# Kernel tuning notes

Hardware: AMD Instinct MI355X
Metric: run time of the kernel (lower is better)

Reference implementation:

```python
import jax, jax.numpy as jnp
import numpy as np

B, T, D, H = 2, 2048, 1024, 16
DK = D // H


def setup_inputs() -> dict:
    key = jax.random.key(0)
    ks = jax.random.split(key, 13)
    s = 1.0 / np.sqrt(D)
    return {
        "q": jax.random.normal(ks[0], (B, T, D), jnp.float32),
        "k": jax.random.normal(ks[1], (B, T, D), jnp.float32),
        "v": jax.random.normal(ks[2], (B, T, D), jnp.float32),
        "mask": jax.random.randint(ks[3], (B, T, T), 0, 2, jnp.int32),
        "Wq": jax.random.normal(ks[4], (D, D), jnp.float32) * s,
        "bq": jax.random.normal(ks[5], (D,), jnp.float32) * s,
        "Wk": jax.random.normal(ks[6], (D, D), jnp.float32) * s,
        "bk": jax.random.normal(ks[7], (D,), jnp.float32) * s,
        "Wv": jax.random.normal(ks[8], (D, D), jnp.float32) * s,
        "bv": jax.random.normal(ks[9], (D,), jnp.float32) * s,
        "Wo": jax.random.normal(ks[10], (D, D), jnp.float32) * s,
        "bo": jax.random.normal(ks[11], (D,), jnp.float32) * s,
    }


def reference(q, k, v, mask, Wq, bq, Wk, bk, Wv, bv, Wo, bo):
    # Linear projections (torch Linear: x @ W.T + b), split into heads.
    Q = (q @ Wq.T + bq).reshape(B, T, H, DK).transpose(0, 2, 1, 3)  # [B,H,Tq,dk]
    K = (k @ Wk.T + bk).reshape(B, T, H, DK).transpose(0, 2, 1, 3)
    V = (v @ Wv.T + bv).reshape(B, T, H, DK).transpose(0, 2, 1, 3)
    scores = jnp.einsum("bhqd,bhkd->bhqk", Q, K) / jnp.sqrt(jnp.float32(DK))
    # 3-dim mask path: mask==0 -> -1e9, broadcast over heads.
    scores = jnp.where(mask[:, None, :, :] == 0, jnp.float32(-1e9), scores)
    attn = jax.nn.softmax(scores, axis=-1)
    out = jnp.einsum("bhqk,bhkd->bhqd", attn, V)  # [B,H,Tq,dk]
    out = out.transpose(0, 2, 1, 3).reshape(B, T, D)
    return out @ Wo.T + bo
```

## Files before the change

### kernel.cpp

```cpp
#include <hip/hip_runtime.h>
#include <cstdint>
#include <cstddef>

#define TSEQ 2048
#define DMOD 1024
#define NHEAD 16
#define NBATCH 2
#define MT (NBATCH * TSEQ)
#define LOG2E 1.44269504088896340736f

typedef __attribute__((ext_vector_type(8))) __bf16 bf16x8;
typedef __attribute__((ext_vector_type(4))) float f32x4;
typedef __attribute__((ext_vector_type(8))) unsigned short u16x8;
typedef __attribute__((ext_vector_type(4))) unsigned short u16x4;
typedef __attribute__((ext_vector_type(4))) uint32_t u32x4;

__device__ __forceinline__ unsigned short f2bf(float f) {
  uint32_t u = __builtin_bit_cast(uint32_t, f);
  u += 0x7fffu + ((u >> 16) & 1u);
  return (unsigned short)(u >> 16);
}

__device__ __forceinline__ uint32_t cvt_pk_bf16(float a, float b) {
  uint32_t r;
  asm("v_cvt_pk_bf16_f32 %0, %1, %2" : "=v"(r) : "v"(a), "v"(b));
  return r;
}

__device__ __forceinline__ void gload_lds16(const void* g, const void* l) {
  auto gp = (const __attribute__((address_space(1))) uint32_t*)((uintptr_t)g);
  auto lp = (__attribute__((address_space(3))) uint32_t*)((uintptr_t)l);
  __builtin_amdgcn_global_load_lds(gp, lp, 16, 0, 0);
}

__global__ __launch_bounds__(256) void cvt_wm(const float* __restrict__ w0,
                                              const float* __restrict__ w1,
                                              const float* __restrict__ w2,
                                              const float* __restrict__ w3,
                                              const int* __restrict__ m,
                                              unsigned short* __restrict__ dw,
                                              uint32_t* __restrict__ mx) {
  const int bx = blockIdx.x;
  if (bx < 4096) {
    const size_t idx = ((size_t)bx * 256 + threadIdx.x) * 4;
    const int wsel = (int)(idx >> 20);
    const float* s = wsel == 0 ? w0 : (wsel == 1 ? w1 : (wsel == 2 ? w2 : w3));
    const float4 t = *(const float4*)(s + (idx & 0xFFFFFu));
    u16x4 o;
    o[0] = f2bf(t.x); o[1] = f2bf(t.y); o[2] = f2bf(t.z); o[3] = f2bf(t.w);
    *(u16x4*)(dw + idx) = o;
  } else {
    const size_t W = (size_t)(bx - 4096) * 256 + threadIdx.x;
    const int hi = (int)((W >> 3) & 3), ct = (int)(W & 7);
    const size_t bqkt = W >> 5;
    const int kt = (int)(bqkt & 15);
    const size_t bq = bqkt >> 4;
    const int4 mm = *(const int4*)(m + bq * TSEQ + kt * 128 + ct * 16 + hi * 4);
    const uint32_t o = (mm.x ? 0xFFu : 0u) | (mm.y ? 0xFF00u : 0u) |
                       (mm.z ? 0xFF0000u : 0u) | (mm.w ? 0xFF000000u : 0u);
    mx[W] = o;
  }
}

__device__ __forceinline__ void store_c(unsigned short* C, size_t idx, float v) { C[idx] = f2bf(v); }
__device__ __forceinline__ void store_c(float* C, size_t idx, float v) { C[idx] = v; }

template <typename OT, int MF, bool AF32>
__global__ __launch_bounds__(256) void gemm_bt(const void* __restrict__ A0v,
                                               const void* __restrict__ A1v,
                                               const void* __restrict__ A2v,
                                               const unsigned short* __restrict__ W0,
                                               const unsigned short* __restrict__ W1,
                                               const unsigned short* __restrict__ W2,
                                               const float* __restrict__ b0,
                                               const float* __restrict__ b1,
                                               const float* __restrict__ b2,
                                               OT* __restrict__ C0, OT* __restrict__ C1, OT* __restrict__ C2,
                                               float s0, float s1, float s2) {
  constexpr int BM = MF * 32;
  constexpr int NX = 4096 / BM;
  const int nb = gridDim.x, per = nb >> 3, bid = blockIdx.x;
  const int swz = (bid & 7) * per + (bid >> 3);
  const int z = swz / (NX * 8);
  const int rem = swz % (NX * 8);
  const int m0 = (rem >> 3) * BM, n0 = (rem & 7) * 128;

  const void* Av = z == 0 ? A0v : (z == 1 ? A1v : A2v);
  const unsigned short* Bw = z == 0 ? W0 : (z == 1 ? W1 : W2);
  const float* bias = z == 0 ? b0 : (z == 1 ? b1 : b2);
  OT* C = z == 0 ? C0 : (z == 1 ? C1 : C2);
  const float scale = z == 0 ? s0 : (z == 1 ? s1 : s2);

  __shared__ alignas(16) unsigned short As[2][BM * 64];
  __shared__ alignas(16) unsigned short Bs[2][128 * 64];
  const int tid = threadIdx.x;
  const int wid = tid >> 6;
  const int lane = tid & 63;
  const int lo = lane & 15, hi = lane >> 4;
  const int wr = wid >> 1, wc = wid & 1;
  f32x4 acc[MF][4] = {};

  float4 fa[MF][2];

  auto loadA = [&](int k0) {
    if constexpr (AF32) {
#pragma unroll
      for (int j = 0; j < MF; ++j) {
        const int chunk = j * 256 + tid;
        const int row = chunk >> 3, cl = (chunk & 7) ^ (row & 7);
        const float* p = (const float*)Av + (size_t)(m0 + row) * DMOD + k0 + cl * 8;
        fa[j][0] = *(const float4*)p;
        fa[j][1] = *(const float4*)(p + 4);
      }
    }
  };
  auto writeA = [&](int buf) {
    if constexpr (AF32) {
#pragma unroll
      for (int j = 0; j < MF; ++j) {
        const int chunk = j * 256 + tid;
        u32x4 o;
        o[0] = cvt_pk_bf16(fa[j][0].x, fa[j][0].y);
        o[1] = cvt_pk_bf16(fa[j][0].z, fa[j][0].w);
        o[2] = cvt_pk_bf16(fa[j][1].x, fa[j][1].y);
        o[3] = cvt_pk_bf16(fa[j][1].z, fa[j][1].w);
        *(u32x4*)((char*)As + buf * (BM * 128) + chunk * 16) = o;
      }
    }
  };
  auto stage = [&](int buf, int k0) {
    if constexpr (!AF32) {
#pragma unroll
      for (int i = 0; i < MF; ++i) {
        const int chunk = i * 256 + tid;
        const int row = chunk >> 3, cl = (chunk & 7) ^ (row & 7);
        gload_lds16((const unsigned short*)Av + (size_t)(m0 + row) * DMOD + k0 + cl * 8,
                    (const char*)As + buf * (BM * 128) + chunk * 16);
      }
    }
#pragma unroll
    for (int i = 0; i < 4; ++i) {
      const int chunk = i * 256 + tid;
      const int row = chunk >> 3, cl = (chunk & 7) ^ (row & 7);
      gload_lds16(Bw + (size_t)(n0 + row) * DMOD + k0 + cl * 8,
                  (const char*)Bs + buf * 16384 + chunk * 16);
    }
  };

  loadA(0);
  writeA(0);
  stage(0, 0);
  __syncthreads();

  for (int k0 = 0; k0 < DMOD; k0 += 64) {
    const int cur = (k0 >> 6) & 1;
    const bool more = k0 + 64 < DMOD;
    if (more) { loadA(k0 + 64); stage(cur ^ 1, k0 + 64); }

#pragma unroll
    for (int kk = 0; kk < 2; ++kk) {
      bf16x8 af[MF], bfr[4];
#pragma unroll
      for (int m = 0; m < MF; ++m) {
        const int row = wr * (MF * 16) + m * 16 + lo;
        af[m] = *(const bf16x8*)((const char*)As + cur * (BM * 128) +
                                 row * 128 + (((kk * 4 + hi) ^ (lo & 7)) * 16));
      }
#pragma unroll
      for (int n = 0; n < 4; ++n) {
        const int row = wc * 64 + n * 16 + lo;
        bfr[n] = *(const bf16x8*)((const char*)Bs + cur * 16384 +
                                  row * 128 + (((kk * 4 + hi) ^ (lo & 7)) * 16));
      }
#pragma unroll
      for (int m = 0; m < MF; ++m)
#pragma unroll
        for (int n = 0; n < 4; ++n)
          acc[m][n] = __builtin_amdgcn_mfma_f32_16x16x32_bf16(af[m], bfr[n], acc[m][n], 0, 0, 0);
    }

    if (more) writeA(cur ^ 1);
    __syncthreads();
  }

#pragma unroll
  for (int n = 0; n < 4; ++n) {
    const int col = n0 + wc * 64 + n * 16 + lo;
    const float bv = bias[col];
#pragma unroll
    for (int m = 0; m < MF; ++m) {
      const int row = m0 + wr * (MF * 16) + m * 16 + hi * 4;
#pragma unroll
      for (int r = 0; r < 4; ++r)
        store_c(C, (size_t)(row + r) * DMOD + col, (acc[m][n][r] + bv) * scale);
    }
  }
}

__global__ __launch_bounds__(256) void transpose_v(const unsigned short* __restrict__ Vp,
                                                   unsigned short* __restrict__ Vt) {
  __shared__ alignas(16) unsigned short tile[64][72];
  const int tid = threadIdx.x;
  const int bt0 = blockIdx.x * 64;
  const int h = blockIdx.y;
  const int b = bt0 >> 11;
  const int t0 = bt0 & (TSEQ - 1);
#pragma unroll
  for (int i = 0; i < 2; ++i) {
    const int chunk = i * 256 + tid;
    const int row = chunk >> 3, c = chunk & 7;
    *(uint4*)((char*)&tile[row][0] + c * 16) =
        *(const uint4*)(Vp + (size_t)(bt0 + row) * DMOD + h * 64 + c * 8);
  }
  __syncthreads();
#pragma unroll
  for (int i = 0; i < 2; ++i) {
    const int chunk = i * 256 + tid;
    const int dk = chunk >> 3, c = chunk & 7;
    u16x8 o;
#pragma unroll
    for (int j = 0; j < 8; ++j) {
      const int x = c * 8 + j;
      const int kl = (x & 32) | ((x & 24) >> 1) | ((x & 4) << 2) | (x & 3);
      o[j] = tile[kl][dk];
    }
    *(u16x8*)(Vt + ((size_t)(b * NHEAD + h) * 64 + dk) * TSEQ + t0 + c * 8) = o;
  }
}

__global__ __launch_bounds__(512, 4) void attn_kernel(const unsigned short* __restrict__ Qp,
                                                      const unsigned short* __restrict__ Kp,
                                                      const unsigned short* __restrict__ Vt,
                                                      const uint32_t* __restrict__ mx,
                                                      unsigned short* __restrict__ AO) {
  __shared__ alignas(16) unsigned short Ks[2][128 * 64];
  __shared__ alignas(16) unsigned short Vs[2][64 * 128];
  const int tid = threadIdx.x;
  const int w = tid >> 6, lane = tid & 63;
  const int lo = lane & 15, hi = lane >> 4;
  const int f = blockIdx.x;
  const int swz = (f & 7) * 64 + (f >> 3);
  const int q0 = (swz & 15) * 128;
  const int h = (swz >> 4) & 15;
  const int b = swz >> 8;

  bf16x8 qf[2];
  {
    const unsigned short* qsrc =
        Qp + (size_t)(b * TSEQ + q0 + w * 16 + lo) * DMOD + h * 64 + hi * 8;
    qf[0] = *(const bf16x8*)qsrc;
    qf[1] = *(const bf16x8*)(qsrc + 32);
  }

  bf16x8 ones;
  {
    u32x4 od;
    od[0] = 0x3F803F80u; od[1] = 0x3F803F80u; od[2] = 0x3F803F80u; od[3] = 0x3F803F80u;
    ones = __builtin_bit_cast(bf16x8, od);
  }

  f32x4 o_acc[4] = {};
  f32x4 l_acc = {};

  const size_t kbase = (size_t)(b * TSEQ) * DMOD + h * 64;
  const size_t vbase = (size_t)(b * NHEAD + h) * 64 * TSEQ;

  const int c0 = tid, c1 = 512 + tid;
  const unsigned short* kp0 = Kp + kbase + (size_t)(c0 >> 3) * DMOD + ((c0 & 7) ^ ((c0 >> 3) & 7)) * 8;
  const unsigned short* kp1 = Kp + kbase + (size_t)(c1 >> 3) * DMOD + ((c1 & 7) ^ ((c1 >> 3) & 7)) * 8;
  const unsigned short* vp0 = Vt + vbase + (size_t)(c0 >> 4) * TSEQ + ((c0 & 15) ^ ((c0 >> 4) & 7)) * 8;
  const unsigned short* vp1 = Vt + vbase + (size_t)(c1 >> 4) * TSEQ + ((c1 & 15) ^ ((c1 >> 4) & 7)) * 8;
  const uint32_t* mp = mx + (size_t)(b * TSEQ + q0 + w * 16 + lo) * 512 + hi * 8;
  const int wb0 = c0 * 16, wb1 = c1 * 16;

  int koffA[8], koffB[8];
#pragma unroll
  for (int ct = 0; ct < 8; ++ct) {
    const int kcol = ct * 16 + lo;
    koffA[ct] = kcol * 128 + ((hi ^ (kcol & 7)) * 16);
    koffB[ct] = kcol * 128 + (((4 + hi) ^ (kcol & 7)) * 16);
  }
  int voff[4][4];
#pragma unroll
  for (int vt = 0; vt < 4; ++vt) {
    const int dk = vt * 16 + lo;
#pragma unroll
    for (int c = 0; c < 4; ++c) voff[vt][c] = dk * 256 + (((c * 4 + hi) ^ (dk & 7)) * 16);
  }

  auto stage = [&](int buf) {
    gload_lds16(kp0, (const char*)Ks[buf] + wb0);
    gload_lds16(kp1, (const char*)Ks[buf] + wb1);
    gload_lds16(vp0, (const char*)Vs[buf] + wb0);
    gload_lds16(vp1, (const char*)Vs[buf] + wb1);
    kp0 += (size_t)128 * DMOD; kp1 += (size_t)128 * DMOD;
    vp0 += 128; vp1 += 128;
  };

  const uint32_t selA = 0x01010000u, selB = 0x03030202u;
  const int NT = TSEQ / 128;

  uint4 mc0 = *(const uint4*)mp, mc1 = *(const uint4*)(mp + 4);
  mp += 32;
  stage(0);
  __syncthreads();

  for (int kt = 0; kt < NT; ++kt) {
    uint4 mn0 = mc0, mn1 = mc1;
    if (kt + 1 < NT) {
      mn0 = *(const uint4*)mp;
      mn1 = *(const uint4*)(mp + 4);
      mp += 32;
      stage((kt + 1) & 1);
    }

    const char* ksb = (const char*)Ks[kt & 1];
    const char* vsb = (const char*)Vs[kt & 1];
    f32x4 s[8];
    __builtin_amdgcn_s_setprio(1);
#pragma unroll
    for (int ct = 0; ct < 8; ++ct) {
      bf16x8 kf0 = *(const bf16x8*)(ksb + koffA[ct]);
      bf16x8 kf1 = *(const bf16x8*)(ksb + koffB[ct]);
      f32x4 zz = {0.f, 0.f, 0.f, 0.f};
      s[ct] = __builtin_amdgcn_mfma_f32_16x16x32_bf16(kf0, qf[0], zz, 0, 0, 0);
      s[ct] = __builtin_amdgcn_mfma_f32_16x16x32_bf16(kf1, qf[1], s[ct], 0, 0, 0);
    }
    __builtin_amdgcn_s_setprio(0);

#pragma unroll
    for (int ct = 0; ct < 8; ++ct) {
      s[ct][0] = __builtin_exp2f(s[ct][0]);
      s[ct][1] = __builtin_exp2f(s[ct][1]);
      s[ct][2] = __builtin_exp2f(s[ct][2]);
      s[ct][3] = __builtin_exp2f(s[ct][3]);
    }

    bf16x8 pf[4];
#pragma unroll
    for (int c = 0; c < 4; ++c) {
      const uint32_t We = c == 0 ? mc0.x : (c == 1 ? mc0.z : (c == 2 ? mc1.x : mc1.z));
      const uint32_t Wo = c == 0 ? mc0.y : (c == 1 ? mc0.w : (c == 2 ? mc1.y : mc1.w));
      u32x4 pd;
      pd[0] = cvt_pk_bf16(s[2 * c][0], s[2 * c][1]) & __builtin_amdgcn_perm(We, We, selA);
      pd[1] = cvt_pk_bf16(s[2 * c][2], s[2 * c][3]) & __builtin_amdgcn_perm(We, We, selB);
      pd[2] = cvt_pk_bf16(s[2 * c + 1][0], s[2 * c + 1][1]) & __builtin_amdgcn_perm(Wo, Wo, selA);
      pd[3] = cvt_pk_bf16(s[2 * c + 1][2], s[2 * c + 1][3]) & __builtin_amdgcn_perm(Wo, Wo, selB);
      pf[c] = __builtin_bit_cast(bf16x8, pd);
    }

    __builtin_amdgcn_s_setprio(1);
#pragma unroll
    for (int vt = 0; vt < 4; ++vt) {
#pragma unroll
      for (int c = 0; c < 4; ++c) {
        bf16x8 vf = *(const bf16x8*)(vsb + voff[vt][c]);
        o_acc[vt] = __builtin_amdgcn_mfma_f32_16x16x32_bf16(pf[c], vf, o_acc[vt], 0, 0, 0);
      }
    }
#pragma unroll
    for (int c = 0; c < 4; ++c)
      l_acc = __builtin_amdgcn_mfma_f32_16x16x32_bf16(pf[c], ones, l_acc, 0, 0, 0);
    __builtin_amdgcn_s_setprio(0);

    __syncthreads();
    mc0 = mn0; mc1 = mn1;
  }

#pragma unroll
  for (int r = 0; r < 4; ++r) {
    const float rl = 1.0f / l_acc[r];
    const size_t orow = (size_t)(b * TSEQ + q0 + w * 16 + hi * 4 + r) * DMOD + h * 64;
#pragma unroll
    for (int vt = 0; vt < 4; ++vt)
      AO[orow + vt * 16 + lo] = f2bf(o_acc[vt][r] * rl);
  }
}

extern "C" void kernel_launch(void* const* d_in, const int* in_sizes, int n_in,
                              void* d_out, int out_size, void* d_ws, size_t ws_size,
                              hipStream_t stream) {
  const float* q  = (const float*)d_in[0];
  const float* k  = (const float*)d_in[1];
  const float* v  = (const float*)d_in[2];
  const int* mask = (const int*)d_in[3];
  const float* Wq = (const float*)d_in[4];
  const float* bq = (const float*)d_in[5];
  const float* Wk = (const float*)d_in[6];
  const float* bk = (const float*)d_in[7];
  const float* Wv = (const float*)d_in[8];
  const float* bv = (const float*)d_in[9];
  const float* Wo = (const float*)d_in[10];
  const float* bo = (const float*)d_in[11];
  float* out = (float*)d_out;

  char* ws = (char*)d_ws;
  const size_t SZ_BT = (size_t)MT * DMOD * 2;

  unsigned short* Qp  = (unsigned short*)(ws + 0);
  unsigned short* Kp  = (unsigned short*)(ws + SZ_BT);
  unsigned short* Vp  = (unsigned short*)(ws + 2 * SZ_BT);
  unsigned short* Vt  = (unsigned short*)(ws + 3 * SZ_BT);
  unsigned short* Wqb = (unsigned short*)(ws + 4 * SZ_BT);
  uint32_t*       mx  = (uint32_t*)(ws + 5 * SZ_BT);
  unsigned short* AO  = Vp;
  unsigned short* Wob = Wqb + 3 * DMOD * DMOD;

  const int nW = DMOD * DMOD;

  cvt_wm<<<dim3(4096 + (NBATCH * TSEQ * 16 * 32) / 256), 256, 0, stream>>>(
      Wq, Wk, Wv, Wo, mask, Wqb, mx);

  const float qs = 0.125f * LOG2E;
  gemm_bt<unsigned short, 4, true><<<dim3(768), 256, 0, stream>>>(
      q, k, v, Wqb, Wqb + nW, Wqb + 2 * nW, bq, bk, bv, Qp, Kp, Vp, qs, 1.0f, 1.0f);

  transpose_v<<<dim3(MT / 64, NHEAD), 256, 0, stream>>>(Vp, Vt);

  attn_kernel<<<dim3(512), 512, 0, stream>>>(Qp, Kp, Vt, mx, AO);

  gemm_bt<float, 2, false><<<dim3(512), 256, 0, stream>>>(
      AO, AO, AO, Wob, Wob, Wob, bo, bo, bo, out, out, out, 1.0f, 1.0f, 1.0f);
}
```

Baseline: 138.8 us.

## Software-pipeline QK of next tile with softmax/PV of current tile

New measurement: 194.0 us. 1.4x slower.

```diff
diff --git a/kernel.cpp b/kernel.cpp
--- a/kernel.cpp
+++ b/kernel.cpp
@@ -234,7 +234,7 @@
                                                       const uint32_t* __restrict__ mx,
                                                       unsigned short* __restrict__ AO) {
   __shared__ alignas(16) unsigned short Ks[2][128 * 64];
-  __shared__ alignas(16) unsigned short Vs[2][64 * 128];
+  __shared__ alignas(16) unsigned short Vs[3][64 * 128];
   const int tid = threadIdx.x;
   const int w = tid >> 6, lane = tid & 63;
   const int lo = lane & 15, hi = lane >> 4;
@@ -288,84 +288,103 @@
     for (int c = 0; c < 4; ++c) voff[vt][c] = dk * 256 + (((c * 4 + hi) ^ (dk & 7)) * 16);
   }
 
-  auto stage = [&](int buf) {
-    gload_lds16(kp0, (const char*)Ks[buf] + wb0);
-    gload_lds16(kp1, (const char*)Ks[buf] + wb1);
-    gload_lds16(vp0, (const char*)Vs[buf] + wb0);
-    gload_lds16(vp1, (const char*)Vs[buf] + wb1);
+  auto stage = [&](int kbuf, int vbuf) {
+    gload_lds16(kp0, (const char*)Ks[kbuf] + wb0);
+    gload_lds16(kp1, (const char*)Ks[kbuf] + wb1);
+    gload_lds16(vp0, (const char*)Vs[vbuf] + wb0);
+    gload_lds16(vp1, (const char*)Vs[vbuf] + wb1);
     kp0 += (size_t)128 * DMOD; kp1 += (size_t)128 * DMOD;
     vp0 += 128; vp1 += 128;
   };
 
   const uint32_t selA = 0x01010000u, selB = 0x03030202u;
+
+#define QK_TILE(S, KSB) do {                                                  \
+    const char* _k = (KSB);                                                   \
+    __builtin_amdgcn_s_setprio(1);                                            \
+    _Pragma("unroll")                                                         \
+    for (int ct = 0; ct < 8; ++ct) {                                          \
+      bf16x8 kf0 = *(const bf16x8*)(_k + koffA[ct]);                          \
+      bf16x8 kf1 = *(const bf16x8*)(_k + koffB[ct]);                          \
+      f32x4 zz = {0.f, 0.f, 0.f, 0.f};                                        \
+      S[ct] = __builtin_amdgcn_mfma_f32_16x16x32_bf16(kf0, qf[0], zz, 0, 0, 0);    \
+      S[ct] = __builtin_amdgcn_mfma_f32_16x16x32_bf16(kf1, qf[1], S[ct], 0, 0, 0); \
+    }                                                                         \
+    __builtin_amdgcn_s_setprio(0);                                            \
+  } while (0)
+
+#define EXPPV_TILE(S, M0, M1, VSB) do {                                       \
+    const char* _v = (VSB);                                                   \
+    _Pragma("unroll")                                                         \
+    for (int ct = 0; ct < 8; ++ct) {                                          \
+      S[ct][0] = __builtin_exp2f(S[ct][0]);                                   \
+      S[ct][1] = __builtin_exp2f(S[ct][1]);                                   \
+      S[ct][2] = __builtin_exp2f(S[ct][2]);                                   \
+      S[ct][3] = __builtin_exp2f(S[ct][3]);                                   \
+    }                                                                         \
+    bf16x8 pf[4];                                                             \
+    _Pragma("unroll")                                                         \
+    for (int c = 0; c < 4; ++c) {                                             \
+      const uint32_t We = c == 0 ? M0.x : (c == 1 ? M0.z : (c == 2 ? M1.x : M1.z)); \
+      const uint32_t Wo = c == 0 ? M0.y : (c == 1 ? M0.w : (c == 2 ? M1.y : M1.w)); \
+      u32x4 pd;                                                               \
+      pd[0] = cvt_pk_bf16(S[2 * c][0], S[2 * c][1]) & __builtin_amdgcn_perm(We, We, selA); \
+      pd[1] = cvt_pk_bf16(S[2 * c][2], S[2 * c][3]) & __builtin_amdgcn_perm(We, We, selB); \
+      pd[2] = cvt_pk_bf16(S[2 * c + 1][0], S[2 * c + 1][1]) & __builtin_amdgcn_perm(Wo, Wo, selA); \
+      pd[3] = cvt_pk_bf16(S[2 * c + 1][2], S[2 * c + 1][3]) & __builtin_amdgcn_perm(Wo, Wo, selB); \
+      pf[c] = __builtin_bit_cast(bf16x8, pd);                                 \
+    }                                                                         \
+    __builtin_amdgcn_s_setprio(1);                                            \
+    _Pragma("unroll")                                                         \
+    for (int vt = 0; vt < 4; ++vt) {                                          \
+      _Pragma("unroll")                                                       \
+      for (int c = 0; c < 4; ++c) {                                           \
+        bf16x8 vf = *(const bf16x8*)(_v + voff[vt][c]);                       \
+        o_acc[vt] = __builtin_amdgcn_mfma_f32_16x16x32_bf16(pf[c], vf, o_acc[vt], 0, 0, 0); \
+      }                                                                       \
+    }                                                                         \
+    _Pragma("unroll")                                                         \
+    for (int c = 0; c < 4; ++c)                                               \
+      l_acc = __builtin_amdgcn_mfma_f32_16x16x32_bf16(pf[c], ones, l_acc, 0, 0, 0); \
+    __builtin_amdgcn_s_setprio(0);                                            \
+  } while (0)
+
   const int NT = TSEQ / 128;
-
-  uint4 mc0 = *(const uint4*)mp, mc1 = *(const uint4*)(mp + 4);
-  mp += 32;
-  stage(0);
+  f32x4 sA[8], sB[8];
+  uint4 mA0, mA1, mB0, mB1;
+
+  mA0 = *(const uint4*)mp; mA1 = *(const uint4*)(mp + 4); mp += 32;
+  stage(0, 0);
   __syncthreads();
-
-  for (int kt = 0; kt < NT; ++kt) {
-    uint4 mn0 = mc0, mn1 = mc1;
-    if (kt + 1 < NT) {
-      mn0 = *(const uint4*)mp;
-      mn1 = *(const uint4*)(mp + 4);
-      mp += 32;
-      stage((kt + 1) & 1);
-    }
-
-    const char* ksb = (const char*)Ks[kt & 1];
-    const char* vsb = (const char*)Vs[kt & 1];
-    f32x4 s[8];
-    __builtin_amdgcn_s_setprio(1);
-#pragma unroll
-    for (int ct = 0; ct < 8; ++ct) {
-      bf16x8 kf0 = *(const bf16x8*)(ksb + koffA[ct]);
-      bf16x8 kf1 = *(const bf16x8*)(ksb + koffB[ct]);
-      f32x4 zz = {0.f, 0.f, 0.f, 0.f};
-      s[ct] = __builtin_amdgcn_mfma_f32_16x16x32_bf16(kf0, qf[0], zz, 0, 0, 0);
-      s[ct] = __builtin_amdgcn_mfma_f32_16x16x32_bf16(kf1, qf[1], s[ct], 0, 0, 0);
-    }
-    __builtin_amdgcn_s_setprio(0);
-
-#pragma unroll
-    for (int ct = 0; ct < 8; ++ct) {
-      s[ct][0] = __builtin_exp2f(s[ct][0]);
-      s[ct][1] = __builtin_exp2f(s[ct][1]);
-      s[ct][2] = __builtin_exp2f(s[ct][2]);
-      s[ct][3] = __builtin_exp2f(s[ct][3]);
-    }
-
-    bf16x8 pf[4];
-#pragma unroll
-    for (int c = 0; c < 4; ++c) {
-      const uint32_t We = c == 0 ? mc0.x : (c == 1 ? mc0.z : (c == 2 ? mc1.x : mc1.z));
-      const uint32_t Wo = c == 0 ? mc0.y : (c == 1 ? mc0.w : (c == 2 ? mc1.y : mc1.w));
-      u32x4 pd;
-      pd[0] = cvt_pk_bf16(s[2 * c][0], s[2 * c][1]) & __builtin_amdgcn_perm(We, We, selA);
-      pd[1] = cvt_pk_bf16(s[2 * c][2], s[2 * c][3]) & __builtin_amdgcn_perm(We, We, selB);
-      pd[2] = cvt_pk_bf16(s[2 * c + 1][0], s[2 * c + 1][1]) & __builtin_amdgcn_perm(Wo, Wo, selA);
-      pd[3] = cvt_pk_bf16(s[2 * c + 1][2], s[2 * c + 1][3]) & __builtin_amdgcn_perm(Wo, Wo, selB);
-      pf[c] = __builtin_bit_cast(bf16x8, pd);
-    }
-
-    __builtin_amdgcn_s_setprio(1);
-#pragma unroll
-    for (int vt = 0; vt < 4; ++vt) {
-#pragma unroll
-      for (int c = 0; c < 4; ++c) {
-        bf16x8 vf = *(const bf16x8*)(vsb + voff[vt][c]);
-        o_acc[vt] = __builtin_amdgcn_mfma_f32_16x16x32_bf16(pf[c], vf, o_acc[vt], 0, 0, 0);
-      }
-    }
-#pragma unroll
-    for (int c = 0; c < 4; ++c)
-      l_acc = __builtin_amdgcn_mfma_f32_16x16x32_bf16(pf[c], ones, l_acc, 0, 0, 0);
-    __builtin_amdgcn_s_setprio(0);
-
+  mB0 = *(const uint4*)mp; mB1 = *(const uint4*)(mp + 4); mp += 32;
+  stage(1, 1);
+  QK_TILE(sA, (const char*)Ks[0]);
+  __syncthreads();
+
+  for (int kt = 0; kt < NT; kt += 2) {
+    uint4 tA0, tA1;
+    if (kt + 2 < NT) {
+      tA0 = *(const uint4*)mp; tA1 = *(const uint4*)(mp + 4); mp += 32;
+      stage(kt & 1, (kt + 2) % 3);
+    }
+    QK_TILE(sB, (const char*)Ks[(kt + 1) & 1]);
+    EXPPV_TILE(sA, mA0, mA1, (const char*)Vs[kt % 3]);
     __syncthreads();
-    mc0 = mn0; mc1 = mn1;
-  }
+    if (kt + 2 < NT) { mA0 = tA0; mA1 = tA1; }
+
+    uint4 tB0, tB1;
+    if (kt + 3 < NT) {
+      tB0 = *(const uint4*)mp; tB1 = *(const uint4*)(mp + 4); mp += 32;
+      stage((kt + 1) & 1, (kt + 3) % 3);
+    }
+    if (kt + 2 < NT) QK_TILE(sA, (const char*)Ks[(kt + 2) & 1]);
+    EXPPV_TILE(sB, mB0, mB1, (const char*)Vs[(kt + 1) % 3]);
+    __syncthreads();
+    if (kt + 3 < NT) { mB0 = tB0; mB1 = tB1; }
+  }
+
+#undef QK_TILE
+#undef EXPPV_TILE
 
 #pragma unroll
   for (int r = 0; r < 4; ++r) {
```
